# Kernel tuning notes

Measured on AMD Instinct MI355X. Metric: run time of the kernel, lower is better.

The kernel has to match this reference:

```python
import jax, jax.numpy as jnp
import numpy as np

N_WAY = 5
K_SHOT = 1
QUERY = 75          # queries per class -> 375 total
PRJ = 14            # projections per support class
C, H, W = 512, 10, 10
NUM_NODE = H * W
SINK_EPS = 0.05     # entropic regularization (on max-normalized cost)
SINK_ITERS = 50


def setup_inputs() -> dict:
    key = jax.random.key(0)
    k1, k2 = jax.random.split(key)
    n_support = N_WAY * K_SHOT * PRJ
    num_query = N_WAY * QUERY
    feat = jax.random.normal(k1, (n_support + num_query, C, H, W), dtype=jnp.float32)
    label = jax.random.randint(k2, (num_query,), 0, N_WAY)
    return {"feat": feat, "label": label}


def _sinkhorn(cost, r, c, eps=SINK_EPS, iters=SINK_ITERS):
    """Batched entropic OT (log-domain Sinkhorn), replacing the per-pair
    cv2.EMD CPU solve. cost: [..., n, m]; r: [..., n]; c: [..., m].
    r and c each sum to NUM_NODE, so total transported mass is NUM_NODE,
    matching the cv2.EMD flow scale. Scaling the cost by a positive scalar
    does not change the (exact-)OT plan, so we max-normalize per pair for a
    consistent effective regularization."""
    scale = jnp.max(cost, axis=(-1, -2), keepdims=True) + 1e-6
    cost = cost / scale
    log_r = jnp.log(r)
    log_c = jnp.log(c)

    def body(fg, _):
        f, g = fg
        f = eps * (log_r - jax.nn.logsumexp((g[..., None, :] - cost) / eps, axis=-1))
        g = eps * (log_c - jax.nn.logsumexp((f[..., :, None] - cost) / eps, axis=-2))
        return (f, g), None

    init = (jnp.zeros_like(r), jnp.zeros_like(c))
    (f, g), _ = jax.lax.scan(body, init, None, length=iters)
    return jnp.exp((f[..., :, None] + g[..., None, :] - cost) / eps)


def reference(feat, label):
    n_support = N_WAY * K_SHOT * PRJ
    support = feat[:n_support].reshape(N_WAY, PRJ, C, H, W)
    query = feat[n_support:]                       # [nq, C, H, W]
    proto = support.mean(axis=1)                   # [way, C, H, W]
    nq = query.shape[0]

    # --- get_weight_vector: <A_node_feat, global_avg(B)> per (A,B) pair ---
    proto_avg = proto.mean(axis=(2, 3))            # [way, C]
    query_avg = query.mean(axis=(2, 3))            # [nq, C]
    qf = query.reshape(nq, C, NUM_NODE)
    pf = proto.reshape(N_WAY, C, NUM_NODE)
    w1 = jax.nn.relu(jnp.einsum('mcp,nc->mnp', qf, proto_avg)) + 0.001  # [nq, way, N]
    w2 = jax.nn.relu(jnp.einsum('ncp,mc->nmp', pf, query_avg)) + 0.001  # [way, nq, N]

    # --- normalize_feature: subtract channel mean ---
    protoN = proto - proto.mean(axis=1, keepdims=True)
    queryN = query - query.mean(axis=1, keepdims=True)

    # --- similarity map: 1 - squared L2 over channels, per node pair ---
    p = protoN.reshape(N_WAY, C, NUM_NODE).transpose(0, 2, 1)  # [way, N, C]
    q = queryN.reshape(nq, C, NUM_NODE).transpose(0, 2, 1)     # [nq, N, C]
    qn = (q ** 2).sum(-1)                                      # [nq, N]
    pn = (p ** 2).sum(-1)                                      # [way, N]
    cross = jnp.einsum('iac,jbc->ijab', q, p)                  # [nq, way, N, N]
    sqd = qn[:, None, :, None] + pn[None, :, None, :] - 2.0 * cross
    sim = 1.0 - sqd                                            # similarity_map
    cost = sqd                                                 # = 1 - sim

    # --- marginal weights, normalized to sum NUM_NODE (as in emd_inference) ---
    ww1 = jax.nn.relu(w1) + 1e-5
    ww1 = ww1 * (NUM_NODE / ww1.sum(-1, keepdims=True))        # [nq, way, N]
    ww2 = jax.nn.relu(jnp.transpose(w2, (1, 0, 2))) + 1e-5     # weight_2[j,i] -> [nq, way, N]
    ww2 = ww2 * (NUM_NODE / ww2.sum(-1, keepdims=True))

    # --- OT flow (detached, like torch.from_numpy(flow)) ---
    flow = jax.lax.stop_gradient(
        _sinkhorn(jax.lax.stop_gradient(cost), jax.lax.stop_gradient(ww1), jax.lax.stop_gradient(ww2))
    )

    temperature = 12.5 / NUM_NODE
    logits = (sim * flow).sum((-1, -2)) * temperature          # [nq, way]
    log_p_y = jax.nn.log_softmax(logits, axis=1)
    loss = -jnp.take_along_axis(log_p_y, label[:, None], axis=1).mean()
    return (log_p_y, loss)
```

## Files before the change

kernel.cpp:

```cpp
#include <hip/hip_runtime.h>
#include <math.h>

#define NW   5
#define PRJ  14
#define CCH  512
#define PP   100
#define NQ   375
#define NS   70
#define NPAIR (NQ*NW)

#define OFF_PROTO   0
#define OFF_PAVG    256000
#define OFF_QAVG    258560
#define OFF_QSQ     450560
#define OFF_PSQ     488060
#define OFF_LOGITS  488560
#define OFF_PF16    490440

typedef float f32x16 __attribute__((ext_vector_type(16)));
typedef _Float16 f16x2 __attribute__((ext_vector_type(2)));
typedef _Float16 f16x8 __attribute__((ext_vector_type(8)));

__device__ __forceinline__ int SWZ(int n) { return n ^ ((n >> 2) & 7); }

__global__ void k_proto(const float* __restrict__ feat, float* __restrict__ ws) {
    int nc = blockIdx.x;
    int n  = nc >> 9;
    int p  = threadIdx.x;
    float s = 0.f;
    if (p < PP) {
        const float* base = feat + (size_t)((n * PRJ) * CCH) * PP + (size_t)(nc & 511) * PP + p;
        #pragma unroll
        for (int k = 0; k < PRJ; ++k) s += base[(size_t)k * CCH * PP];
        s *= (1.f / PRJ);
        ws[OFF_PROTO + nc * PP + p] = s;
    }
    float v = (p < PP) ? s : 0.f;
    #pragma unroll
    for (int off = 32; off; off >>= 1) v += __shfl_down(v, off);
    __shared__ float red[2];
    if ((threadIdx.x & 63) == 0) red[threadIdx.x >> 6] = v;
    __syncthreads();
    if (threadIdx.x == 0) ws[OFF_PAVG + nc] = (red[0] + red[1]) * (1.f / PP);
}

__global__ __launch_bounds__(256) void k_qstat(const float* __restrict__ src,
                                               float* __restrict__ dst_sq,
                                               float* __restrict__ dst_avg) {
    __shared__ __align__(16) float t[6400];
    int b = blockIdx.x, tid = threadIdx.x;
    const float* base = src + (size_t)b * CCH * PP;
    float qsq = 0.f;
    for (int c0 = 0; c0 < CCH; c0 += 64) {
        __syncthreads();
        const float4* g = (const float4*)(base + (size_t)c0 * PP);
        for (int i = tid; i < 1600; i += 256) ((float4*)t)[i] = g[i];
        __syncthreads();
        if (tid < PP) {
            #pragma unroll 8
            for (int c = 0; c < 64; ++c) { float x = t[c * PP + tid]; qsq = fmaf(x, x, qsq); }
        } else if (tid >= 128 && tid < 192) {
            int ch = tid - 128;
            const float4* row = (const float4*)(t + ch * PP);
            float s = 0.f;
            #pragma unroll
            for (int i = 0; i < 25; ++i) { float4 v = row[i]; s += (v.x + v.y) + (v.z + v.w); }
            if (dst_avg) dst_avg[(size_t)b * CCH + c0 + ch] = s * (1.f / PP);
        }
    }
    if (tid < PP) dst_sq[b * PP + tid] = qsq;
}

__global__ __launch_bounds__(256) void k_pconv(float* __restrict__ ws) {
    int b = blockIdx.x;
    int n = b >> 4, kt = b & 15;
    int tid = threadIdx.x;
    int c0 = kt * 32;
    uint* img = (uint*)(ws + OFF_PF16) + (size_t)b * 2048;
    const float* pb = ws + OFF_PROTO + (size_t)n * CCH * PP;
    const float* pavg = ws + OFF_PAVG + n * CCH;
    for (int i = tid; i < 1600; i += 256) {
        int cp = i / 100, col = i - cp * 100;
        float a0 = pb[(size_t)(c0 + 2 * cp) * PP + col];
        float a1 = pb[(size_t)(c0 + 2 * cp + 1) * PP + col];
        uint pk = __builtin_bit_cast(uint, __builtin_amdgcn_cvt_pkrtz(a0, a1));
        img[(((cp >> 2) << 7) | SWZ(col)) * 4 + (cp & 3)] = pk;
    }
    if (tid < 16) {
        int cp = tid;
        float a0 = pavg[c0 + 2 * cp], a1 = pavg[c0 + 2 * cp + 1];
        uint pk = __builtin_bit_cast(uint, __builtin_amdgcn_cvt_pkrtz(a0, a1));
        img[(((cp >> 2) << 7) | 101) * 4 + (cp & 3)] = pk;
    }
    for (int i = tid; i < 448; i += 256) {
        int dw = i & 3; int t2 = i >> 2;
        int s_i = t2 % 28; int k4 = t2 / 28;
        int s = 100 + s_i;
        if (s == 101) continue;
        img[(((k4) << 7) | s) * 4 + dw] = (s == 100) ? 0x3C003C00u : 0u;
    }
}

__global__ __launch_bounds__(256, 4) void k_pair(const float* __restrict__ query,
                                                 float* __restrict__ ws) {
    __shared__ __align__(16) char SH[22400];
    __shared__ __align__(16) float uvec[112], vvec[112];
    __shared__ float wrL[PP], wcL[PP], qnl[PP], pnl[PP], sqv[PP], spv[PP];
    __shared__ float red[8];

    uint* Kst = (uint*)SH;

    int p_ = blockIdx.x;
    int xcd = p_ & 7, off_ = p_ >> 3;
    int pair = (xcd < 3) ? (xcd * 235 + off_) : (705 + (xcd - 3) * 234 + off_);

    int m = pair / NW;
    int n = pair - m * NW;
    int tid = threadIdx.x;
    int lane = tid & 63, wid = tid >> 6;
    int lrow = lane & 31, lhi = lane >> 5;

    const float* qb = query + (size_t)m * CCH * PP;
    const float* qavg_g = ws + OFF_QAVG + (size_t)m * CCH;
    const uint* pimg = (const uint*)(ws + OFF_PF16) + (size_t)n * 16 * 2048;

    for (int idx = tid; idx < 112; idx += 256) {
        int s_i = idx % 28; int k4 = idx / 28;
        int s = 100 + s_i;
        if (s == 101) continue;
        uint4 val = (s == 100)
                  ? make_uint4(0x3C003C00u, 0x3C003C00u, 0x3C003C00u, 0x3C003C00u)
                  : make_uint4(0u, 0u, 0u, 0u);
        *(uint4*)&SH[(k4 * 128 + s) * 16] = val;
    }

    f32x16 acc[4];
    #pragma unroll
    for (int tc = 0; tc < 4; ++tc)
        #pragma unroll
        for (int e = 0; e < 16; ++e) acc[tc][e] = 0.f;

    int arow16 = SWZ(32 * wid + lrow) * 16;
    int bcol16[4];
    #pragma unroll
    for (int tc = 0; tc < 4; ++tc) bcol16[tc] = SWZ(32 * tc + lrow) * 16;

    for (int kt = 0; kt < 16; ++kt) {
        int c0 = kt * 32;
        for (int idx = tid; idx < 400; idx += 256) {
            int cp = idx / 25, n4 = idx - cp * 25;
            const float* src = qb + (size_t)(c0 + 2 * cp) * PP + n4 * 4;
            float4 x0 = *(const float4*)src;
            float4 x1 = *(const float4*)(src + PP);
            const float* p0 = (const float*)&x0;
            const float* p1 = (const float*)&x1;
            int basedw = ((cp >> 2) << 7);
            int dwb = (cp & 3) * 4;
            #pragma unroll
            for (int i4 = 0; i4 < 4; ++i4) {
                int node = n4 * 4 + i4;
                uint pk = __builtin_bit_cast(uint, __builtin_amdgcn_cvt_pkrtz(p0[i4], p1[i4]));
                *(uint*)&SH[(basedw + SWZ(node)) * 16 + dwb] = pk;
            }
        }
        if (tid < 16) {
            int cp = tid;
            uint pk = __builtin_bit_cast(uint,
                __builtin_amdgcn_cvt_pkrtz(qavg_g[c0 + 2 * cp], qavg_g[c0 + 2 * cp + 1]));
            *(uint*)&SH[(((cp >> 2) << 7) + 101) * 16 + (cp & 3) * 4] = pk;
        }
        {
            const float4* gB = (const float4*)(pimg + (size_t)kt * 2048);
            float4* sB = (float4*)&SH[8192];
            for (int i = tid; i < 512; i += 256) sB[i] = gB[i];
        }
        __syncthreads();
        __builtin_amdgcn_s_setprio(1);
        #pragma unroll
        for (int s = 0; s < 2; ++s) {
            int kb = (2 * s + lhi) * 2048;
            f16x8 ah = *(const f16x8*)&SH[kb + arow16];
            #pragma unroll
            for (int tc = 0; tc < 4; ++tc) {
                f16x8 bh = *(const f16x8*)&SH[8192 + kb + bcol16[tc]];
                acc[tc] = __builtin_amdgcn_mfma_f32_32x32x16_f16(ah, bh, acc[tc], 0, 0, 0);
            }
        }
        __builtin_amdgcn_s_setprio(0);
        __syncthreads();
    }

    if ((lane & 31) == 4 || (lane & 31) == 5) {
        float* dst = ((lane & 31) == 4) ? wrL : sqv;
        #pragma unroll
        for (int reg = 0; reg < 16; ++reg) {
            int row = 32 * wid + (reg & 3) + 8 * (reg >> 2) + 4 * lhi;
            if (row < PP) dst[row] = acc[3][reg];
        }
    }
    if (wid == 3 && lhi == 1) {
        #pragma unroll
        for (int tc = 0; tc < 4; ++tc) {
            int col = 32 * tc + lrow;
            if (col < PP) { wcL[col] = acc[tc][0]; spv[col] = acc[tc][1]; }
        }
    }
    if (tid < 112) vvec[tid] = 1.f;
    __syncthreads();

    float v1 = 0.f, v2 = 0.f;
    if (tid < PP) {
        v1 = fmaxf(wrL[tid], 0.f) + 0.00101f;
        v2 = fmaxf(wcL[tid], 0.f) + 0.00101f;
    }
    float s1 = v1, s2 = v2;
    #pragma unroll
    for (int off = 32; off; off >>= 1) { s1 += __shfl_down(s1, off); s2 += __shfl_down(s2, off); }
    if ((tid & 63) == 0) { red[tid >> 6] = s1; red[4 + (tid >> 6)] = s2; }
    __syncthreads();
    float t1 = red[0] + red[1], t2 = red[4] + red[5];
    if (tid < PP) {
        wrL[tid] = v1 * (100.f / t1) * 32768.f;
        wcL[tid] = v2 * (100.f / t2) * 32768.f;
        float sq = sqv[tid], sp = spv[tid];
        qnl[tid] = ws[OFF_QSQ + m * PP + tid] - sq * sq * (1.f / 512.f);
        pnl[tid] = ws[OFF_PSQ + n * PP + tid] - sp * sp * (1.f / 512.f);
    }
    __syncthreads();

    float spc[4], pnc[4];
    #pragma unroll
    for (int tc = 0; tc < 4; ++tc) {
        int col = 32 * tc + lrow;
        bool cv = col < PP;
        spc[tc] = cv ? spv[col] : 0.f;
        pnc[tc] = cv ? pnl[col] : 0.f;
    }
    float mymax = -1e30f;
    #pragma unroll
    for (int reg = 0; reg < 16; ++reg) {
        int row = 32 * wid + (reg & 3) + 8 * (reg >> 2) + 4 * lhi;
        bool rv = row < PP;
        float sqr = rv ? sqv[row] : 0.f;
        float qnr = rv ? qnl[row] : 0.f;
        #pragma unroll
        for (int tc = 0; tc < 4; ++tc) {
            float sqd = qnr + pnc[tc] - 2.f * (acc[tc][reg] - sqr * spc[tc] * (1.f / 512.f));
            acc[tc][reg] = sqd;
            int col = 32 * tc + lrow;
            if (rv && col < PP) mymax = fmaxf(mymax, sqd);
        }
    }
    #pragma unroll
    for (int off = 32; off; off >>= 1) mymax = fmaxf(mymax, __shfl_down(mymax, off));
    __syncthreads();
    if (lane == 0) red[wid] = mymax;
    __syncthreads();
    float scale = fmaxf(fmaxf(red[0], red[1]), fmaxf(red[2], red[3])) + 1e-6f;
    float k2 = (1.f / scale) * (20.f * 1.44269504088896f);

    #pragma unroll
    for (int tc = 0; tc < 4; ++tc) {
        float kv[16];
        #pragma unroll
        for (int reg = 0; reg < 16; ++reg) kv[reg] = exp2f(fmaf(-acc[tc][reg], k2, 15.f));
        int col = 32 * tc + lrow;
        #pragma unroll
        for (int reg = 0; reg < 16; ++reg) {
            float pv = __shfl_xor(kv[reg], 1);
            int row = 32 * wid + (reg & 3) + 8 * (reg >> 2) + 4 * lhi;
            if (!(lane & 1) && row < PP && col < PP) {
                int j = col >> 1;
                int dw = (j < 25) ? j : (j + 3);
                uint pk = __builtin_bit_cast(uint, __builtin_amdgcn_cvt_pkrtz(kv[reg], pv));
                Kst[row * 56 + dw] = pk;
            }
        }
    }
    __syncthreads();

    int r_ = tid >> 1, hf = tid & 1;
    bool sact = tid < 200;
    int widx = r_ + (r_ >= 50 ? 6 : 0);
    uint Kr[25], KTr[25];
    float wr_own = 0.f, wc_own = 0.f;
    if (sact) {
        const uint* rp = Kst + r_ * 56 + 28 * hf;
        #pragma unroll
        for (int q = 0; q < 25; ++q) Kr[q] = rp[q];
        int j = r_ >> 1;
        int dwc = (j < 25) ? j : (j + 3);
        int sh = (r_ & 1) * 16;
        const uint* cp0 = Kst + (50 * hf) * 56 + dwc;
        #pragma unroll
        for (int q = 0; q < 25; ++q) {
            uint d0 = cp0[(2 * q) * 56];
            uint d1 = cp0[(2 * q + 1) * 56];
            KTr[q] = ((d0 >> sh) & 0xFFFFu) | (((d1 >> sh) & 0xFFFFu) << 16);
        }
        wr_own = wrL[r_];
        wc_own = wcL[r_];
    }
    __syncthreads();

    for (int it = 0; it < 50; ++it) {
        if (sact) {
            const float* vp = vvec + hf * 56;
            float sA = 0.f, sB = 0.f;
            #pragma unroll
            for (int q = 0; q < 25; ++q) {
                f16x2 h = __builtin_bit_cast(f16x2, Kr[q]);
                sA = fmaf((float)h[0], vp[2 * q], sA);
                sB = fmaf((float)h[1], vp[2 * q + 1], sB);
            }
            float s = sA + sB;
            s += __shfl_xor(s, 1);
            if (!hf) uvec[widx] = wr_own * __builtin_amdgcn_rcpf(s);
        }
        __syncthreads();
        if (sact) {
            const float* up = uvec + hf * 56;
            float sA = 0.f, sB = 0.f;
            #pragma unroll
            for (int q = 0; q < 25; ++q) {
                f16x2 h = __builtin_bit_cast(f16x2, KTr[q]);
                sA = fmaf((float)h[0], up[2 * q], sA);
                sB = fmaf((float)h[1], up[2 * q + 1], sB);
            }
            float s = sA + sB;
            s += __shfl_xor(s, 1);
            if (!hf) vvec[widx] = wc_own * __builtin_amdgcn_rcpf(s);
        }
        __syncthreads();
    }

    float lsum = 0.f;
    if (sact) {
        float ur = uvec[widx];
        const float* vp = vvec + hf * 56;
        float rk2 = scale * (1.f / (20.f * 1.44269504088896f));
        #pragma unroll
        for (int q = 0; q < 25; ++q) {
            f16x2 h = __builtin_bit_cast(f16x2, Kr[q]);
            float k0 = (float)h[0], k1 = (float)h[1];
            float sq0 = (15.f - __log2f(k0)) * rk2;
            float sq1 = (15.f - __log2f(k1)) * rk2;
            lsum = fmaf((1.f - sq0) * k0, vp[2 * q], lsum);
            lsum = fmaf((1.f - sq1) * k1, vp[2 * q + 1], lsum);
        }
        lsum *= ur;
    }
    #pragma unroll
    for (int off = 32; off; off >>= 1) lsum += __shfl_down(lsum, off);
    if (lane == 0) red[wid] = lsum;
    __syncthreads();
    if (tid == 0)
        ws[OFF_LOGITS + pair] = ((red[0] + red[1]) + (red[2] + red[3])) * (0.125f / 32768.f);
}

__global__ void k_final(const int* __restrict__ label, const float* __restrict__ ws,
                        float* __restrict__ out) {
    int t = threadIdx.x;
    float contrib = 0.f;
    if (t < NQ) {
        float lg[NW];
        #pragma unroll
        for (int n = 0; n < NW; ++n) lg[n] = ws[OFF_LOGITS + t * NW + n];
        float mx = lg[0];
        #pragma unroll
        for (int n = 1; n < NW; ++n) mx = fmaxf(mx, lg[n]);
        float s = 0.f;
        #pragma unroll
        for (int n = 0; n < NW; ++n) s += expf(lg[n] - mx);
        float lse = mx + logf(s);
        int lab = label[t];
        #pragma unroll
        for (int n = 0; n < NW; ++n) {
            float lp = lg[n] - lse;
            out[t * NW + n] = lp;
            if (n == lab) contrib = -lp;
        }
    }
    #pragma unroll
    for (int off = 32; off; off >>= 1) contrib += __shfl_down(contrib, off);
    __shared__ float red[6];
    if ((t & 63) == 0) red[t >> 6] = contrib;
    __syncthreads();
    if (t == 0) {
        float s = 0.f;
        #pragma unroll
        for (int i = 0; i < 6; ++i) s += red[i];
        out[NQ * NW] = s * (1.f / NQ);
    }
}

extern "C" void kernel_launch(void* const* d_in, const int* in_sizes, int n_in,
                              void* d_out, int out_size, void* d_ws, size_t ws_size,
                              hipStream_t stream) {
    const float* feat  = (const float*)d_in[0];
    const int*   label = (const int*)d_in[1];
    float* out = (float*)d_out;
    float* ws  = (float*)d_ws;
    const float* query = feat + (size_t)NS * CCH * PP;

    k_proto<<<NW * CCH, 128, 0, stream>>>(feat, ws);
    k_qstat<<<NQ, 256, 0, stream>>>(query, ws + OFF_QSQ, ws + OFF_QAVG);
    k_qstat<<<NW, 256, 0, stream>>>(ws + OFF_PROTO, ws + OFF_PSQ, (float*)nullptr);
    k_pconv<<<NW * 16, 256, 0, stream>>>(ws);
    k_pair<<<NPAIR, 256, 0, stream>>>(query, ws);
    k_final<<<1, 384, 0, stream>>>(label, ws, out);
}
```

Measured before the change: 244.1 us.

## Process two query-support pairs per 512-thread block, sharing query tile when possible

```diff
diff --git a/kernel.cpp b/kernel.cpp
--- a/kernel.cpp
+++ b/kernel.cpp
@@ -8,6 +8,7 @@
 #define NQ   375
 #define NS   70
 #define NPAIR (NQ*NW)
+#define NBLK 938
 
 #define OFF_PROTO   0
 #define OFF_PAVG    256000
@@ -101,37 +102,58 @@
     }
 }
 
-__global__ __launch_bounds__(256, 4) void k_pair(const float* __restrict__ query,
+__global__ __launch_bounds__(512, 4) void k_pair(const float* __restrict__ query,
                                                  float* __restrict__ ws) {
-    __shared__ __align__(16) char SH[22400];
-    __shared__ __align__(16) float uvec[112], vvec[112];
-    __shared__ float wrL[PP], wcL[PP], qnl[PP], pnl[PP], sqv[PP], spv[PP];
-    __shared__ float red[8];
-
-    uint* Kst = (uint*)SH;
-
-    int p_ = blockIdx.x;
-    int xcd = p_ & 7, off_ = p_ >> 3;
-    int pair = (xcd < 3) ? (xcd * 235 + off_) : (705 + (xcd - 3) * 234 + off_);
-
-    int m = pair / NW;
-    int n = pair - m * NW;
-    int tid = threadIdx.x;
-    int lane = tid & 63, wid = tid >> 6;
+    __shared__ __align__(16) char SH[51456];
+    float* uvbase = (float*)(SH + 44800);
+    float* stat   = (float*)(SH + 46592);
+    float* red    = (float*)(SH + 51392);
+
+    int b = blockIdx.x;
+    int xcd = b & 7, off_ = b >> 3;
+    int wg = (xcd < 2) ? (xcd * 118 + off_) : (236 + (xcd - 2) * 117 + off_);
+    int p0 = 2 * wg;
+    int p1v = p0 + 1;
+    int p1 = (p1v < NPAIR) ? p1v : p0;
+
+    int tid  = threadIdx.x;
+    int prob = tid >> 8;
+    int ptid = tid & 255;
+    int lane = tid & 63;
+    int wid  = (tid >> 6) & 3;
     int lrow = lane & 31, lhi = lane >> 5;
 
-    const float* qb = query + (size_t)m * CCH * PP;
-    const float* qavg_g = ws + OFF_QAVG + (size_t)m * CCH;
-    const uint* pimg = (const uint*)(ws + OFF_PF16) + (size_t)n * 16 * 2048;
-
-    for (int idx = tid; idx < 112; idx += 256) {
-        int s_i = idx % 28; int k4 = idx / 28;
+    int m0 = p0 / NW, m1 = p1 / NW;
+    int n0 = p0 - m0 * NW, n1 = p1 - m1 * NW;
+    bool sharedA = (m0 == m1);
+    int mp = prob ? m1 : m0;
+    int np = prob ? n1 : n0;
+    int aslot = sharedA ? 0 : prob;
+
+    const float* qb     = query + (size_t)mp * CCH * PP;
+    const float* qavg_g = ws + OFF_QAVG + (size_t)mp * CCH;
+    const uint*  pimg   = (const uint*)(ws + OFF_PF16) + (size_t)np * 16 * 2048;
+
+    uint*  Kst  = (uint*)(SH + prob * 22400);
+    float* uvec = uvbase + prob * 224;
+    float* vvec = uvec + 112;
+    float* wrP  = stat + prob * 100;
+    float* wcP  = stat + 200 + prob * 100;
+    float* qnlP = stat + 400 + prob * 100;
+    float* sqvP = stat + 600 + prob * 100;
+    float* pnlP = stat + 800 + prob * 100;
+    float* spvP = stat + 1000 + prob * 100;
+
+    for (int idx = tid; idx < 224; idx += 512) {
+        int slot = idx / 112;
+        int t2 = idx - slot * 112;
+        int s_i = t2 % 28, k4 = t2 / 28;
         int s = 100 + s_i;
         if (s == 101) continue;
         uint4 val = (s == 100)
                   ? make_uint4(0x3C003C00u, 0x3C003C00u, 0x3C003C00u, 0x3C003C00u)
                   : make_uint4(0u, 0u, 0u, 0u);
-        *(uint4*)&SH[(k4 * 128 + s) * 16] = val;
+        *(uint4*)&SH[slot * 8192 + (k4 * 128 + s) * 16] = val;
     }
 
     f32x16 acc[4];
@@ -147,42 +169,62 @@
 
     for (int kt = 0; kt < 16; ++kt) {
         int c0 = kt * 32;
-        for (int idx = tid; idx < 400; idx += 256) {
-            int cp = idx / 25, n4 = idx - cp * 25;
-            const float* src = qb + (size_t)(c0 + 2 * cp) * PP + n4 * 4;
-            float4 x0 = *(const float4*)src;
-            float4 x1 = *(const float4*)(src + PP);
-            const float* p0 = (const float*)&x0;
-            const float* p1 = (const float*)&x1;
-            int basedw = ((cp >> 2) << 7);
-            int dwb = (cp & 3) * 4;
-            #pragma unroll
-            for (int i4 = 0; i4 < 4; ++i4) {
-                int node = n4 * 4 + i4;
-                uint pk = __builtin_bit_cast(uint, __builtin_amdgcn_cvt_pkrtz(p0[i4], p1[i4]));
-                *(uint*)&SH[(basedw + SWZ(node)) * 16 + dwb] = pk;
-            }
-        }
-        if (tid < 16) {
-            int cp = tid;
+        if (sharedA) {
+            for (int idx = tid; idx < 400; idx += 512) {
+                int cp = idx / 25, n4 = idx - cp * 25;
+                const float* src = qb + (size_t)(c0 + 2 * cp) * PP + n4 * 4;
+                float4 x0 = *(const float4*)src;
+                float4 x1 = *(const float4*)(src + PP);
+                const float* q0 = (const float*)&x0;
+                const float* q1 = (const float*)&x1;
+                int basedw = ((cp >> 2) << 7);
+                int dwb = (cp & 3) * 4;
+                #pragma unroll
+                for (int i4 = 0; i4 < 4; ++i4) {
+                    int node = n4 * 4 + i4;
+                    uint pk = __builtin_bit_cast(uint, __builtin_amdgcn_cvt_pkrtz(q0[i4], q1[i4]));
+                    *(uint*)&SH[(basedw + SWZ(node)) * 16 + dwb] = pk;
+                }
+            }
+        } else {
+            for (int idx = ptid; idx < 400; idx += 256) {
+                int cp = idx / 25, n4 = idx - cp * 25;
+                const float* src = qb + (size_t)(c0 + 2 * cp) * PP + n4 * 4;
+                float4 x0 = *(const float4*)src;
+                float4 x1 = *(const float4*)(src + PP);
+                const float* q0 = (const float*)&x0;
+                const float* q1 = (const float*)&x1;
+                int basedw = ((cp >> 2) << 7);
+                int dwb = (cp & 3) * 4;
+                #pragma unroll
+                for (int i4 = 0; i4 < 4; ++i4) {
+                    int node = n4 * 4 + i4;
+                    uint pk = __builtin_bit_cast(uint, __builtin_amdgcn_cvt_pkrtz(q0[i4], q1[i4]));
+                    *(uint*)&SH[prob * 8192 + (basedw + SWZ(node)) * 16 + dwb] = pk;
+                }
+            }
+        }
+        if (sharedA ? (tid < 16) : (ptid < 16)) {
+            int cp = sharedA ? tid : ptid;
             uint pk = __builtin_bit_cast(uint,
                 __builtin_amdgcn_cvt_pkrtz(qavg_g[c0 + 2 * cp], qavg_g[c0 + 2 * cp + 1]));
-            *(uint*)&SH[(((cp >> 2) << 7) + 101) * 16 + (cp & 3) * 4] = pk;
+            int slot = sharedA ? 0 : prob;
+            *(uint*)&SH[slot * 8192 + (((cp >> 2) << 7) + 101) * 16 + (cp & 3) * 4] = pk;
         }
         {
             const float4* gB = (const float4*)(pimg + (size_t)kt * 2048);
-            float4* sB = (float4*)&SH[8192];
-            for (int i = tid; i < 512; i += 256) sB[i] = gB[i];
+            float4* sB = (float4*)&SH[16384 + prob * 8192];
+            for (int i = ptid; i < 512; i += 256) sB[i] = gB[i];
         }
         __syncthreads();
         __builtin_amdgcn_s_setprio(1);
         #pragma unroll
         for (int s = 0; s < 2; ++s) {
             int kb = (2 * s + lhi) * 2048;
-            f16x8 ah = *(const f16x8*)&SH[kb + arow16];
+            f16x8 ah = *(const f16x8*)&SH[aslot * 8192 + kb + arow16];
             #pragma unroll
             for (int tc = 0; tc < 4; ++tc) {
-                f16x8 bh = *(const f16x8*)&SH[8192 + kb + bcol16[tc]];
+                f16x8 bh = *(const f16x8*)&SH[16384 + prob * 8192 + kb + bcol16[tc]];
                 acc[tc] = __builtin_amdgcn_mfma_f32_32x32x16_f16(ah, bh, acc[tc], 0, 0, 0);
             }
         }
@@ -191,7 +233,7 @@
     }
 
     if ((lane & 31) == 4 || (lane & 31) == 5) {
-        float* dst = ((lane & 31) == 4) ? wrL : sqv;
+        float* dst = ((lane & 31) == 4) ? wrP : sqvP;
         #pragma unroll
         for (int reg = 0; reg < 16; ++reg) {
             int row = 32 * wid + (reg & 3) + 8 * (reg >> 2) + 4 * lhi;
@@ -202,29 +244,30 @@
         #pragma unroll
         for (int tc = 0; tc < 4; ++tc) {
             int col = 32 * tc + lrow;
-            if (col < PP) { wcL[col] = acc[tc][0]; spv[col] = acc[tc][1]; }
-        }
-    }
-    if (tid < 112) vvec[tid] = 1.f;
+            if (col < PP) { wcP[col] = acc[tc][0]; spvP[col] = acc[tc][1]; }
+        }
+    }
+    if (ptid < 112) vvec[ptid] = 1.f;
     __syncthreads();
 
     float v1 = 0.f, v2 = 0.f;
-    if (tid < PP) {
-        v1 = fmaxf(wrL[tid], 0.f) + 0.00101f;
-        v2 = fmaxf(wcL[tid], 0.f) + 0.00101f;
+    if (ptid < PP) {
+        v1 = fmaxf(wrP[ptid], 0.f) + 0.00101f;
+        v2 = fmaxf(wcP[ptid], 0.f) + 0.00101f;
     }
     float s1 = v1, s2 = v2;
     #pragma unroll
     for (int off = 32; off; off >>= 1) { s1 += __shfl_down(s1, off); s2 += __shfl_down(s2, off); }
-    if ((tid & 63) == 0) { red[tid >> 6] = s1; red[4 + (tid >> 6)] = s2; }
-    __syncthreads();
-    float t1 = red[0] + red[1], t2 = red[4] + red[5];
-    if (tid < PP) {
-        wrL[tid] = v1 * (100.f / t1) * 32768.f;
-        wcL[tid] = v2 * (100.f / t2) * 32768.f;
-        float sq = sqv[tid], sp = spv[tid];
-        qnl[tid] = ws[OFF_QSQ + m * PP + tid] - sq * sq * (1.f / 512.f);
-        pnl[tid] = ws[OFF_PSQ + n * PP + tid] - sp * sp * (1.f / 512.f);
+    if (lane == 0) { red[prob * 4 + wid] = s1; red[8 + prob * 4 + wid] = s2; }
+    __syncthreads();
+    float t1 = red[prob * 4] + red[prob * 4 + 1];
+    float t2 = red[8 + prob * 4] + red[8 + prob * 4 + 1];
+    if (ptid < PP) {
+        wrP[ptid] = v1 * (100.f / t1) * 32768.f;
+        wcP[ptid] = v2 * (100.f / t2) * 32768.f;
+        float sq = sqvP[ptid], sp = spvP[ptid];
+        qnlP[ptid] = ws[OFF_QSQ + mp * PP + ptid] - sq * sq * (1.f / 512.f);
+        pnlP[ptid] = ws[OFF_PSQ + np * PP + ptid] - sp * sp * (1.f / 512.f);
     }
     __syncthreads();
 
@@ -233,16 +276,16 @@
     for (int tc = 0; tc < 4; ++tc) {
         int col = 32 * tc + lrow;
         bool cv = col < PP;
-        spc[tc] = cv ? spv[col] : 0.f;
-        pnc[tc] = cv ? pnl[col] : 0.f;
+        spc[tc] = cv ? spvP[col] : 0.f;
+        pnc[tc] = cv ? pnlP[col] : 0.f;
     }
     float mymax = -1e30f;
     #pragma unroll
     for (int reg = 0; reg < 16; ++reg) {
         int row = 32 * wid + (reg & 3) + 8 * (reg >> 2) + 4 * lhi;
         bool rv = row < PP;
-        float sqr = rv ? sqv[row] : 0.f;
-        float qnr = rv ? qnl[row] : 0.f;
+        float sqr = rv ? sqvP[row] : 0.f;
+        float qnr = rv ? qnlP[row] : 0.f;
         #pragma unroll
         for (int tc = 0; tc < 4; ++tc) {
             float sqd = qnr + pnc[tc] - 2.f * (acc[tc][reg] - sqr * spc[tc] * (1.f / 512.f));
@@ -254,9 +297,10 @@
     #pragma unroll
     for (int off = 32; off; off >>= 1) mymax = fmaxf(mymax, __shfl_down(mymax, off));
     __syncthreads();
-    if (lane == 0) red[wid] = mymax;
-    __syncthreads();
-    float scale = fmaxf(fmaxf(red[0], red[1]), fmaxf(red[2], red[3])) + 1e-6f;
+    if (lane == 0) red[prob * 4 + wid] = mymax;
+    __syncthreads();
+    float scale = fmaxf(fmaxf(red[prob * 4], red[prob * 4 + 1]),
+                        fmaxf(red[prob * 4 + 2], red[prob * 4 + 3])) + 1e-6f;
     float k2 = (1.f / scale) * (20.f * 1.44269504088896f);
 
     #pragma unroll
@@ -279,8 +323,8 @@
     }
     __syncthreads();
 
-    int r_ = tid >> 1, hf = tid & 1;
-    bool sact = tid < 200;
+    int r_ = ptid >> 1, hf = ptid & 1;
+    bool sact = ptid < 200;
     int widx = r_ + (r_ >= 50 ? 6 : 0);
     uint Kr[25], KTr[25];
     float wr_own = 0.f, wc_own = 0.f;
@@ -298,36 +342,56 @@
             uint d1 = cp0[(2 * q + 1) * 56];
             KTr[q] = ((d0 >> sh) & 0xFFFFu) | (((d1 >> sh) & 0xFFFFu) << 16);
         }
-        wr_own = wrL[r_];
-        wc_own = wcL[r_];
+        wr_own = wrP[r_];
+        wc_own = wcP[r_];
     }
     __syncthreads();
 
     for (int it = 0; it < 50; ++it) {
         if (sact) {
-            const float* vp = vvec + hf * 56;
-            float sA = 0.f, sB = 0.f;
+            const float*  vp  = vvec + hf * 56;
+            const float4* vp4 = (const float4*)vp;
+            float a0 = 0.f, a1 = 0.f, a2 = 0.f, a3 = 0.f;
             #pragma unroll
-            for (int q = 0; q < 25; ++q) {
-                f16x2 h = __builtin_bit_cast(f16x2, Kr[q]);
-                sA = fmaf((float)h[0], vp[2 * q], sA);
-                sB = fmaf((float)h[1], vp[2 * q + 1], sB);
-            }
-            float s = sA + sB;
+            for (int j = 0; j < 12; ++j) {
+                float4 V = vp4[j];
+                f16x2 hA = __builtin_bit_cast(f16x2, Kr[2 * j]);
+                f16x2 hB = __builtin_bit_cast(f16x2, Kr[2 * j + 1]);
+                a0 = fmaf((float)hA[0], V.x, a0);
+                a1 = fmaf((float)hA[1], V.y, a1);
+                a2 = fmaf((float)hB[0], V.z, a2);
+                a3 = fmaf((float)hB[1], V.w, a3);
+            }
+            {
+                f16x2 hT = __builtin_bit_cast(f16x2, Kr[24]);
+                a0 = fmaf((float)hT[0], vp[48], a0);
+                a1 = fmaf((float)hT[1], vp[49], a1);
+            }
+            float s = (a0 + a1) + (a2 + a3);
             s += __shfl_xor(s, 1);
             if (!hf) uvec[widx] = wr_own * __builtin_amdgcn_rcpf(s);
         }
         __syncthreads();
         if (sact) {
-            const float* up = uvec + hf * 56;
-            float sA = 0.f, sB = 0.f;
+            const float*  up  = uvec + hf * 56;
+            const float4* up4 = (const float4*)up;
+            float a0 = 0.f, a1 = 0.f, a2 = 0.f, a3 = 0.f;
             #pragma unroll
-            for (int q = 0; q < 25; ++q) {
-                f16x2 h = __builtin_bit_cast(f16x2, KTr[q]);
-                sA = fmaf((float)h[0], up[2 * q], sA);
-                sB = fmaf((float)h[1], up[2 * q + 1], sB);
-            }
-            float s = sA + sB;
+            for (int j = 0; j < 12; ++j) {
+                float4 U = up4[j];
+                f16x2 hA = __builtin_bit_cast(f16x2, KTr[2 * j]);
+                f16x2 hB = __builtin_bit_cast(f16x2, KTr[2 * j + 1]);
+                a0 = fmaf((float)hA[0], U.x, a0);
+                a1 = fmaf((float)hA[1], U.y, a1);
+                a2 = fmaf((float)hB[0], U.z, a2);
+                a3 = fmaf((float)hB[1], U.w, a3);
+            }
+            {
+                f16x2 hT = __builtin_bit_cast(f16x2, KTr[24]);
+                a0 = fmaf((float)hT[0], up[48], a0);
+                a1 = fmaf((float)hT[1], up[49], a1);
+            }
+            float s = (a0 + a1) + (a2 + a3);
             s += __shfl_xor(s, 1);
             if (!hf) vvec[widx] = wc_own * __builtin_amdgcn_rcpf(s);
         }
@@ -352,10 +416,12 @@
     }
     #pragma unroll
     for (int off = 32; off; off >>= 1) lsum += __shfl_down(lsum, off);
-    if (lane == 0) red[wid] = lsum;
+    if (lane == 0) red[prob * 4 + wid] = lsum;
     __syncthreads();
     if (tid == 0)
-        ws[OFF_LOGITS + pair] = ((red[0] + red[1]) + (red[2] + red[3])) * (0.125f / 32768.f);
+        ws[OFF_LOGITS + p0] = ((red[0] + red[1]) + (red[2] + red[3])) * (0.125f / 32768.f);
+    if (tid == 256 && p1v < NPAIR)
+        ws[OFF_LOGITS + p1] = ((red[4] + red[5]) + (red[6] + red[7])) * (0.125f / 32768.f);
 }
 
 __global__ void k_final(const int* __restrict__ label, const float* __restrict__ ws,
@@ -407,6 +473,6 @@
     k_qstat<<<NQ, 256, 0, stream>>>(query, ws + OFF_QSQ, ws + OFF_QAVG);
     k_qstat<<<NW, 256, 0, stream>>>(ws + OFF_PROTO, ws + OFF_PSQ, (float*)nullptr);
     k_pconv<<<NW * 16, 256, 0, stream>>>(ws);
-    k_pair<<<NPAIR, 256, 0, stream>>>(query, ws);
+    k_pair<<<NBLK, 512, 0, stream>>>(query, ws);
     k_final<<<1, 384, 0, stream>>>(label, ws, out);
 }
```

Result: no change. 247.6 us (+1.5%).

## Store Sinkhorn scaling vectors as packed fp16 and use fdot2 matvecs

Applied to the files above, without the earlier changes.

```diff
diff --git a/kernel.cpp b/kernel.cpp
--- a/kernel.cpp
+++ b/kernel.cpp
@@ -104,7 +104,7 @@
 __global__ __launch_bounds__(256, 4) void k_pair(const float* __restrict__ query,
                                                  float* __restrict__ ws) {
     __shared__ __align__(16) char SH[22400];
-    __shared__ __align__(16) float uvec[112], vvec[112];
+    __shared__ __align__(16) uint uh[56], vh[56];
     __shared__ float wrL[PP], wcL[PP], qnl[PP], pnl[PP], sqv[PP], spv[PP];
     __shared__ float red[8];
 
@@ -205,7 +205,10 @@
             if (col < PP) { wcL[col] = acc[tc][0]; spv[col] = acc[tc][1]; }
         }
     }
-    if (tid < 112) vvec[tid] = 1.f;
+    if (tid < 56) {
+        vh[tid] = (tid < 25 || (tid >= 28 && tid < 53)) ? 0x3C003C00u : 0u;
+        uh[tid] = 0u;
+    }
     __syncthreads();
 
     float v1 = 0.f, v2 = 0.f;
@@ -220,8 +223,8 @@
     __syncthreads();
     float t1 = red[0] + red[1], t2 = red[4] + red[5];
     if (tid < PP) {
-        wrL[tid] = v1 * (100.f / t1) * 32768.f;
-        wcL[tid] = v2 * (100.f / t2) * 32768.f;
+        wrL[tid] = v1 * (100.f / t1) * 4.f;
+        wcL[tid] = v2 * (100.f / t2) * 4.f;
         float sq = sqv[tid], sp = spv[tid];
         qnl[tid] = ws[OFF_QSQ + m * PP + tid] - sq * sq * (1.f / 512.f);
         pnl[tid] = ws[OFF_PSQ + n * PP + tid] - sp * sp * (1.f / 512.f);
@@ -281,7 +284,6 @@
 
     int r_ = tid >> 1, hf = tid & 1;
     bool sact = tid < 200;
-    int widx = r_ + (r_ >= 50 ? 6 : 0);
     uint Kr[25], KTr[25];
     float wr_own = 0.f, wc_own = 0.f;
     if (sact) {
@@ -303,59 +305,75 @@
     }
     __syncthreads();
 
+    int tpk = tid >> 2;
+    float u_ = 0.f, v_ = 0.f;
     for (int it = 0; it < 50; ++it) {
         if (sact) {
-            const float* vp = vvec + hf * 56;
-            float sA = 0.f, sB = 0.f;
-            #pragma unroll
-            for (int q = 0; q < 25; ++q) {
-                f16x2 h = __builtin_bit_cast(f16x2, Kr[q]);
-                sA = fmaf((float)h[0], vp[2 * q], sA);
-                sB = fmaf((float)h[1], vp[2 * q + 1], sB);
-            }
-            float s = sA + sB;
+            uint4 vv[7];
+            const uint4* vp4 = (const uint4*)(vh + hf * 28);
+            #pragma unroll
+            for (int i = 0; i < 7; ++i) vv[i] = vp4[i];
+            const uint* vw = (const uint*)vv;
+            float s = 0.f;
+            #pragma unroll
+            for (int q = 0; q < 25; ++q)
+                s = __builtin_amdgcn_fdot2(__builtin_bit_cast(f16x2, Kr[q]),
+                                           __builtin_bit_cast(f16x2, vw[q]), s, false);
             s += __shfl_xor(s, 1);
-            if (!hf) uvec[widx] = wr_own * __builtin_amdgcn_rcpf(s);
+            u_ = fminf(wr_own * __builtin_amdgcn_rcpf(s), 60000.f);
+        }
+        {
+            float u_nb = __shfl_down(u_, 2);
+            if (sact && (tid & 3) == 0)
+                uh[tpk + (tpk >= 25 ? 3 : 0)] =
+                    __builtin_bit_cast(uint, __builtin_amdgcn_cvt_pkrtz(u_, u_nb));
         }
         __syncthreads();
         if (sact) {
-            const float* up = uvec + hf * 56;
-            float sA = 0.f, sB = 0.f;
-            #pragma unroll
-            for (int q = 0; q < 25; ++q) {
-                f16x2 h = __builtin_bit_cast(f16x2, KTr[q]);
-                sA = fmaf((float)h[0], up[2 * q], sA);
-                sB = fmaf((float)h[1], up[2 * q + 1], sB);
-            }
-            float s = sA + sB;
+            uint4 uu[7];
+            const uint4* up4 = (const uint4*)(uh + hf * 28);
+            #pragma unroll
+            for (int i = 0; i < 7; ++i) uu[i] = up4[i];
+            const uint* uw = (const uint*)uu;
+            float s = 0.f;
+            #pragma unroll
+            for (int q = 0; q < 25; ++q)
+                s = __builtin_amdgcn_fdot2(__builtin_bit_cast(f16x2, KTr[q]),
+                                           __builtin_bit_cast(f16x2, uw[q]), s, false);
             s += __shfl_xor(s, 1);
-            if (!hf) vvec[widx] = wc_own * __builtin_amdgcn_rcpf(s);
+            v_ = fminf(wc_own * __builtin_amdgcn_rcpf(s), 60000.f);
+        }
+        {
+            float v_nb = __shfl_down(v_, 2);
+            if (sact && (tid & 3) == 0)
+                vh[tpk + (tpk >= 25 ? 3 : 0)] =
+                    __builtin_bit_cast(uint, __builtin_amdgcn_cvt_pkrtz(v_, v_nb));
         }
         __syncthreads();
     }
 
     float lsum = 0.f;
     if (sact) {
-        float ur = uvec[widx];
-        const float* vp = vvec + hf * 56;
+        const uint* vp = vh + hf * 28;
         float rk2 = scale * (1.f / (20.f * 1.44269504088896f));
         #pragma unroll
         for (int q = 0; q < 25; ++q) {
             f16x2 h = __builtin_bit_cast(f16x2, Kr[q]);
+            f16x2 vv = __builtin_bit_cast(f16x2, vp[q]);
             float k0 = (float)h[0], k1 = (float)h[1];
             float sq0 = (15.f - __log2f(k0)) * rk2;
             float sq1 = (15.f - __log2f(k1)) * rk2;
-            lsum = fmaf((1.f - sq0) * k0, vp[2 * q], lsum);
-            lsum = fmaf((1.f - sq1) * k1, vp[2 * q + 1], lsum);
-        }
-        lsum *= ur;
+            lsum = fmaf((1.f - sq0) * k0, (float)vv[0], lsum);
+            lsum = fmaf((1.f - sq1) * k1, (float)vv[1], lsum);
+        }
+        lsum *= u_;
     }
     #pragma unroll
     for (int off = 32; off; off >>= 1) lsum += __shfl_down(lsum, off);
     if (lane == 0) red[wid] = lsum;
     __syncthreads();
     if (tid == 0)
-        ws[OFF_LOGITS + pair] = ((red[0] + red[1]) + (red[2] + red[3])) * (0.125f / 32768.f);
+        ws[OFF_LOGITS + pair] = ((red[0] + red[1]) + (red[2] + red[3])) * (0.125f / 4.f);
 }
 
 __global__ void k_final(const int* __restrict__ label, const float* __restrict__ ws,
```

Measured after the change: 233.7 us. 1.04x faster.
